# Kernel tuning notes

Hardware: AMD Instinct MI355X
Metric: run time of the kernel (lower is better)

Reference implementation:

```python
import jax, jax.numpy as jnp
import numpy as np

HIDDEN = 1152
NUM_HEADS = 16
HEAD_DIM = HIDDEN // NUM_HEADS  # 72
BATCH, SEQ = 8, 1024


def setup_inputs() -> dict:
    key = jax.random.key(0)
    ks = jax.random.split(key, 9)
    s = 0.02
    return {
        "x": jax.random.normal(ks[0], (BATCH, SEQ, HIDDEN), dtype=jnp.float32),
        "wq": jax.random.normal(ks[1], (HIDDEN, HIDDEN), dtype=jnp.float32) * s,
        "bq": jax.random.normal(ks[2], (HIDDEN,), dtype=jnp.float32) * s,
        "wk": jax.random.normal(ks[3], (HIDDEN, HIDDEN), dtype=jnp.float32) * s,
        "bk": jax.random.normal(ks[4], (HIDDEN,), dtype=jnp.float32) * s,
        "wv": jax.random.normal(ks[5], (HIDDEN, HIDDEN), dtype=jnp.float32) * s,
        "bv": jax.random.normal(ks[6], (HIDDEN,), dtype=jnp.float32) * s,
        "wo": jax.random.normal(ks[7], (HIDDEN, HIDDEN), dtype=jnp.float32) * s,
        "bo": jax.random.normal(ks[8], (HIDDEN,), dtype=jnp.float32) * s,
    }


def reference(x, wq, bq, wk, bk, wv, bv, wo, bo):
    B, S, H = x.shape
    nh, hd = NUM_HEADS, HEAD_DIM
    # projections (weights stored [in, out] to match nn.Linear x @ W^T with W^T precomposed)
    q = (x @ wq + bq).reshape(B, S, nh, hd).transpose(0, 2, 1, 3)  # [B,nh,S,hd]
    k = (x @ wk + bk).reshape(B, S, nh, hd).transpose(0, 2, 1, 3)
    v = (x @ wv + bv).reshape(B, S, nh, hd).transpose(0, 2, 1, 3)
    scale = 1.0 / jnp.sqrt(jnp.asarray(hd, dtype=x.dtype))
    scores = jnp.einsum("bhqd,bhkd->bhqk", q, k) * scale  # [B,nh,S,S]
    attn = jax.nn.softmax(scores, axis=-1)
    out = jnp.einsum("bhqk,bhkd->bhqd", attn, v)  # [B,nh,S,hd]
    out = out.transpose(0, 2, 1, 3).reshape(B, S, H)
    return out @ wo + bo
```

## Files before the change

### kernel.cpp

```cpp
#include <hip/hip_runtime.h>
#include <hip/hip_bf16.h>

#define HIDDEN 1152
#define NUM_HEADS 16
#define BATCH 8
#define SEQ 1024
#define MROWS (BATCH * SEQ)
#define KSTRIDE 104
#define QSCALE_L2E (0.11785113019775793f * 1.4426950408889634f)

typedef __attribute__((ext_vector_type(8))) short short8;
typedef __attribute__((ext_vector_type(4))) float f32x4;

__device__ inline short f2bf(float x) {
  unsigned u = __float_as_uint(x);
  unsigned r = (u + 0x7FFFu + ((u >> 16) & 1u)) >> 16;
  return (short)(r & 0xFFFFu);
}

__device__ inline float fexp2(float x) { return __builtin_exp2f(x); }

__device__ inline void gload16(const void* g, void* l) {
  __builtin_amdgcn_global_load_lds(
      (const __attribute__((address_space(1))) void*)g,
      (__attribute__((address_space(3))) void*)l, 16, 0, 0);
}

__global__ __launch_bounds__(256) void k_prep(const float* __restrict__ X,
                                              short* __restrict__ Xb,
                                              short* __restrict__ Kp,
                                              short* __restrict__ Vt) {
  const int bid = blockIdx.x;
  if (bid < 4608) {
    const size_t base = ((size_t)bid * 256 + threadIdx.x) * 8;
    float4 a = *(const float4*)(X + base);
    float4 b = *(const float4*)(X + base + 4);
    short8 o = {f2bf(a.x), f2bf(a.y), f2bf(a.z), f2bf(a.w),
                f2bf(b.x), f2bf(b.y), f2bf(b.z), f2bf(b.w)};
    *(short8*)(Xb + base) = o;
  } else if (bid < 5120) {
    const int r = (bid - 4608) * 256 + threadIdx.x;
    const short8 z0 = {(short)0xC100, 0, 0, 0, 0, 0, 0, 0};
    const short8 z = {0, 0, 0, 0, 0, 0, 0, 0};
    short* p = Kp + (size_t)r * KSTRIDE + 72;
    *(short8*)(p) = z0;
    *(short8*)(p + 8) = z;
    *(short8*)(p + 16) = z;
  } else {
    const int t = (bid - 5120) * 256 + threadIdx.x;
    const int bh = t >> 10;
    const int off = (t & 1023) * 8;
    const short o = ((t & 1023) >> 7) == 0 ? (short)0x3F80 : (short)0;
    short8 v = {o, o, o, o, o, o, o, o};
    *(short8*)(Vt + (size_t)bh * 81920 + 73728 + off) = v;
  }
}

__global__ __launch_bounds__(256) void k_cvtw(const float* __restrict__ W0,
                                              const float* __restrict__ W1,
                                              const float* __restrict__ W2,
                                              const float* __restrict__ W3,
                                              short* __restrict__ Wt) {
  __shared__ float T[64][65];
  const float* W = (blockIdx.z == 0) ? W0 : (blockIdx.z == 1) ? W1
                 : (blockIdx.z == 2) ? W2 : W3;
  short* dst = Wt + (size_t)blockIdx.z * HIDDEN * HIDDEN;
  const int n0 = blockIdx.x * 64, k0 = blockIdx.y * 64;
  const int tid = threadIdx.x;
  for (int t = tid; t < 4096; t += 256) {
    int r = t >> 6, c = t & 63;
    T[r][c] = W[(size_t)(k0 + r) * HIDDEN + n0 + c];
  }
  __syncthreads();
  for (int t = tid; t < 4096; t += 256) {
    int r = t >> 6, c = t & 63;
    dst[(size_t)(n0 + r) * HIDDEN + k0 + c] = f2bf(T[c][r]);
  }
}

__global__ __launch_bounds__(512) void k_gemm_qkv(
    const short* __restrict__ A, const short* __restrict__ Bt,
    const float* __restrict__ bq, const float* __restrict__ bk,
    const float* __restrict__ bv, short* __restrict__ Qb,
    short* __restrict__ Kp, short* __restrict__ Vt) {
  __shared__ __align__(16) short SM[24576];
  short* As = SM;
  short* Bs = SM + 16384;
  const int tid = threadIdx.x;
  const int lane = tid & 63;
  const int wid = tid >> 6;
  const int wr = wid >> 1, wc = wid & 1;
  const int flat = blockIdx.y * 27 + blockIdx.x;
  const int rid = (flat & 7) * 108 + (flat >> 3);
  const int row0 = (rid / 27) << 8;
  const int colTile = rid % 27;
  const int col0 = colTile << 7;
  const int l15 = lane & 15, lh = lane >> 4;
  const int lr8 = lane >> 3;
  const int csrc = ((lane & 7) ^ lr8) << 3;

  const f32x4 fz = {0.f, 0.f, 0.f, 0.f};
  f32x4 acc[4][4];
#pragma unroll
  for (int m = 0; m < 4; ++m)
#pragma unroll
    for (int n = 0; n < 4; ++n) acc[m][n] = fz;

  for (int k0 = 0; k0 < HIDDEN; k0 += 64) {
#pragma unroll
    for (int i = 0; i < 4; ++i) {
      const int c = (wid << 2) + i;
      const int r = (c << 3) + lr8;
      gload16(A + (size_t)(row0 + r) * HIDDEN + k0 + csrc, (void*)(As + (c << 9)));
    }
#pragma unroll
    for (int i = 0; i < 2; ++i) {
      const int c = (wid << 1) + i;
      const int r = (c << 3) + lr8;
      gload16(Bt + (size_t)(col0 + r) * HIDDEN + k0 + csrc, (void*)(Bs + (c << 9)));
    }
    __syncthreads();
#pragma unroll
    for (int ks = 0; ks < 2; ++ks) {
      short8 af[4], bfr[4];
#pragma unroll
      for (int m = 0; m < 4; ++m) {
        const int r = (wr << 6) + (m << 4) + l15;
        const int off = ((ks << 6) + (lh << 4)) ^ ((r & 7) << 4);
        af[m] = *(const short8*)((const char*)As + r * 128 + off);
      }
#pragma unroll
      for (int n = 0; n < 4; ++n) {
        const int r = (wc << 6) + (n << 4) + l15;
        const int off = ((ks << 6) + (lh << 4)) ^ ((r & 7) << 4);
        bfr[n] = *(const short8*)((const char*)Bs + r * 128 + off);
      }
      __builtin_amdgcn_s_setprio(1);
#pragma unroll
      for (int m = 0; m < 4; ++m)
#pragma unroll
        for (int n = 0; n < 4; ++n)
          acc[m][n] = __builtin_amdgcn_mfma_f32_16x16x32_bf16(af[m], bfr[n], acc[m][n], 0, 0, 0);
      __builtin_amdgcn_s_setprio(0);
    }
    __syncthreads();
  }

  const int cseg = colTile / 9;
  const int cwithin = (colTile % 9) << 7;
  if (cseg < 2) {
    short* dst = (cseg == 0) ? Qb : Kp;
    const float* bias = (cseg == 0) ? bq : bk;
    const float scl = (cseg == 0) ? QSCALE_L2E : 1.0f;
    const int rstride = (cseg == 0) ? 72 : KSTRIDE;
#pragma unroll
    for (int n = 0; n < 4; ++n) {
      const int c = cwithin + (wc << 6) + (n << 4) + l15;
      const int h = c / 72;
      const int d = c - h * 72;
      const float bvx = bias[c];
#pragma unroll
      for (int m = 0; m < 4; ++m)
#pragma unroll
        for (int i = 0; i < 4; ++i) {
          const int r = row0 + (wr << 6) + (m << 4) + (lh << 2) + i;
          const int b = r >> 10, s = r & 1023;
          dst[(size_t)((((b << 4) + h) << 10) + s) * rstride + d] =
              f2bf((acc[m][n][i] + bvx) * scl);
        }
    }
  } else {
    const int b = row0 >> 10;
    const int sb = row0 & 1023;
    short* Td = SM;
#pragma unroll
    for (int p = 0; p < 2; ++p) {
      if (wc == p) {
#pragma unroll
        for (int n = 0; n < 4; ++n) {
          const int ci = n * 16 + l15;
          const float bvx = bv[cwithin + p * 64 + ci];
#pragma unroll
          for (int m = 0; m < 4; ++m) {
            const int r0 = (wr << 6) + (m << 4) + (lh << 2);
            short4 o;
            o.x = f2bf(acc[m][n][0] + bvx);
            o.y = f2bf(acc[m][n][1] + bvx);
            o.z = f2bf(acc[m][n][2] + bvx);
            o.w = f2bf(acc[m][n][3] + bvx);
            *(short4*)(Td + ci * 264 + r0) = o;
          }
        }
      }
      __syncthreads();
      {
        const int ci = tid >> 3;
        const int part = tid & 7;
        const int cg = cwithin + p * 64 + ci;
        const int h = cg / 72;
        const int d = cg - h * 72;
        short* dstp = Vt + (((size_t)(((b << 4) + h) * 80 + d)) << 10) + sb + part * 32;
        const short* srcp = Td + ci * 264 + part * 32;
#pragma unroll
        for (int k = 0; k < 4; ++k)
          *(short8*)(dstp + k * 8) = *(const short8*)(srcp + k * 8);
      }
      __syncthreads();
    }
  }
}

__global__ __launch_bounds__(512) void k_gemm_o(const short* __restrict__ A,
                                                const short* __restrict__ Bt,
                                                const float* __restrict__ bias,
                                                float* __restrict__ C) {
  __shared__ __align__(16) short SM[24576];
  short* As = SM;
  short* Bs = SM + 16384;
  const int tid = threadIdx.x;
  const int lane = tid & 63;
  const int wid = tid >> 6;
  const int wr = wid >> 1, wc = wid & 1;
  const int flat = blockIdx.y * 9 + blockIdx.x;
  const int rid = (flat & 7) * 36 + (flat >> 3);
  const int row0 = (rid / 9) << 8;
  const int col0 = (rid % 9) << 7;
  const int l15 = lane & 15, lh = lane >> 4;
  const int lr8 = lane >> 3;
  const int csrc = ((lane & 7) ^ lr8) << 3;

  const f32x4 fz = {0.f, 0.f, 0.f, 0.f};
  f32x4 acc[4][4];
#pragma unroll
  for (int m = 0; m < 4; ++m)
#pragma unroll
    for (int n = 0; n < 4; ++n) acc[m][n] = fz;

  for (int k0 = 0; k0 < HIDDEN; k0 += 64) {
#pragma unroll
    for (int i = 0; i < 4; ++i) {
      const int c = (wid << 2) + i;
      const int r = (c << 3) + lr8;
      gload16(A + (size_t)(row0 + r) * HIDDEN + k0 + csrc, (void*)(As + (c << 9)));
    }
#pragma unroll
    for (int i = 0; i < 2; ++i) {
      const int c = (wid << 1) + i;
      const int r = (c << 3) + lr8;
      gload16(Bt + (size_t)(col0 + r) * HIDDEN + k0 + csrc, (void*)(Bs + (c << 9)));
    }
    __syncthreads();
#pragma unroll
    for (int ks = 0; ks < 2; ++ks) {
      short8 af[4], bfr[4];
#pragma unroll
      for (int m = 0; m < 4; ++m) {
        const int r = (wr << 6) + (m << 4) + l15;
        const int off = ((ks << 6) + (lh << 4)) ^ ((r & 7) << 4);
        af[m] = *(const short8*)((const char*)As + r * 128 + off);
      }
#pragma unroll
      for (int n = 0; n < 4; ++n) {
        const int r = (wc << 6) + (n << 4) + l15;
        const int off = ((ks << 6) + (lh << 4)) ^ ((r & 7) << 4);
        bfr[n] = *(const short8*)((const char*)Bs + r * 128 + off);
      }
      __builtin_amdgcn_s_setprio(1);
#pragma unroll
      for (int m = 0; m < 4; ++m)
#pragma unroll
        for (int n = 0; n < 4; ++n)
          acc[m][n] = __builtin_amdgcn_mfma_f32_16x16x32_bf16(af[m], bfr[n], acc[m][n], 0, 0, 0);
      __builtin_amdgcn_s_setprio(0);
    }
    __syncthreads();
  }

#pragma unroll
  for (int n = 0; n < 4; ++n) {
    const int c = col0 + (wc << 6) + (n << 4) + l15;
    const float bvx = bias[c];
#pragma unroll
    for (int m = 0; m < 4; ++m)
#pragma unroll
      for (int i = 0; i < 4; ++i) {
        const int r = row0 + (wr << 6) + (m << 4) + (lh << 2) + i;
        C[(size_t)r * HIDDEN + c] = acc[m][n][i] + bvx;
      }
  }
}

__global__ __launch_bounds__(512, 4) void k_attn(const short* __restrict__ Qg,
                                                 const short* __restrict__ Kp,
                                                 const short* __restrict__ Vt,
                                                 short* __restrict__ Og) {
  __shared__ __align__(16) short Ks[64 * KSTRIDE];
  __shared__ __align__(16) short Vs[80 * 64];
  __shared__ __align__(16) short Ps[8 * 16 * 72];
  const int tid = threadIdx.x, lane = tid & 63, wid = tid >> 6;
  const int l15 = lane & 15, lh = lane >> 4;
  const int id = blockIdx.x;
  const int rid = (id & 7) * 64 + (id >> 3);
  const int bh = rid >> 2;
  const int q0 = (rid & 3) << 8;
  const short8 sz = {0, 0, 0, 0, 0, 0, 0, 0};
  const f32x4 fz = {0.f, 0.f, 0.f, 0.f};

  short8 qf[2][3];
#pragma unroll
  for (int m = 0; m < 2; ++m)
#pragma unroll
    for (int ks = 0; ks < 3; ++ks) {
      const int row = q0 + wid * 32 + m * 16 + l15;
      const int e0 = ks * 32 + lh * 8;
      if (e0 < 72)
        qf[m][ks] = *(const short8*)(Qg + ((size_t)bh * 1024 + row) * 72 + e0);
      else if (e0 == 72) {
        short8 v = sz;
        v[0] = (short)0x3F80;
        qf[m][ks] = v;
      } else
        qf[m][ks] = sz;
    }

  f32x4 oacc[2][5];
#pragma unroll
  for (int m = 0; m < 2; ++m)
#pragma unroll
    for (int no = 0; no < 5; ++no) oacc[m][no] = fz;

  const char* kgb = (const char*)Kp + ((size_t)bh * 1024) * (KSTRIDE * 2);
  const char* vgb = (const char*)Vt + (size_t)bh * 163840;
  short* psw = Ps + wid * 1152;

  for (int kt = 0; kt < 16; ++kt) {
    const char* kg = kgb + (size_t)kt * 64 * (KSTRIDE * 2);
    for (int c = wid; c < 13; c += 8)
      gload16(kg + c * 1024 + lane * 16, (char*)Ks + c * 1024);
    for (int c = wid; c < 10; c += 8) {
      const int p = c * 1024 + lane * 16;
      const int d = p >> 7;
      const int sc16 = (lane & 7) ^ (d & 7);
      gload16(vgb + (size_t)d * 2048 + kt * 128 + sc16 * 16, (char*)Vs + c * 1024);
    }
    __syncthreads();

#pragma unroll
    for (int m = 0; m < 2; ++m) {
      f32x4 sa[4];
#pragma unroll
      for (int n = 0; n < 4; ++n) sa[n] = fz;
#pragma unroll
      for (int ks = 0; ks < 3; ++ks) {
        short8 kf[4];
#pragma unroll
        for (int n = 0; n < 4; ++n)
          kf[n] = *(const short8*)((const char*)Ks + (n * 16 + l15) * 208 + ks * 64 + lh * 16);
        __builtin_amdgcn_s_setprio(1);
#pragma unroll
        for (int n = 0; n < 4; ++n)
          sa[n] = __builtin_amdgcn_mfma_f32_16x16x32_bf16(kf[n], qf[m][ks], sa[n], 0, 0, 0);
        __builtin_amdgcn_s_setprio(0);
      }

#pragma unroll
      for (int n = 0; n < 4; ++n)
#pragma unroll
        for (int i = 0; i < 4; ++i) sa[n][i] = fexp2(sa[n][i]);

#pragma unroll
      for (int n = 0; n < 4; ++n) {
        unsigned w0 = __builtin_amdgcn_perm(__float_as_uint(sa[n][1]),
                                            __float_as_uint(sa[n][0]), 0x07060302u);
        unsigned w1 = __builtin_amdgcn_perm(__float_as_uint(sa[n][3]),
                                            __float_as_uint(sa[n][2]), 0x07060302u);
        uint2 w = {w0, w1};
        *(uint2*)((char*)psw + l15 * 144 + n * 32 + lh * 8) = w;
      }

#pragma unroll
      for (int ks = 0; ks < 2; ++ks) {
        const short8 pa = *(const short8*)((const char*)psw + l15 * 144 + ks * 64 + lh * 16);
        short8 vb[5];
        const int cc = ((ks << 2) + lh) ^ (l15 & 7);
#pragma unroll
        for (int no = 0; no < 5; ++no)
          vb[no] = *(const short8*)((const char*)Vs + no * 2048 + l15 * 128 + cc * 16);
        __builtin_amdgcn_s_setprio(1);
#pragma unroll
        for (int no = 0; no < 5; ++no)
          oacc[m][no] = __builtin_amdgcn_mfma_f32_16x16x32_bf16(pa, vb[no], oacc[m][no], 0, 0, 0);
        __builtin_amdgcn_s_setprio(0);
      }
    }
    __syncthreads();
  }

  const int b = bh >> 4, h = bh & 15;
#pragma unroll
  for (int m = 0; m < 2; ++m) {
    float inv[4];
#pragma unroll
    for (int i = 0; i < 4; ++i)
      inv[i] = 1.0f / __shfl(oacc[m][4][i], (lane & 48) + 8);
#pragma unroll
    for (int no = 0; no < 5; ++no) {
      const int d = no * 16 + l15;
      if (d < 72) {
#pragma unroll
        for (int i = 0; i < 4; ++i) {
          const int s = q0 + wid * 32 + m * 16 + lh * 4 + i;
          Og[((size_t)(b * 1024 + s)) * HIDDEN + h * 72 + d] = f2bf(oacc[m][no][i] * inv[i]);
        }
      }
    }
  }
}

extern "C" void kernel_launch(void* const* d_in, const int* in_sizes, int n_in,
                              void* d_out, int out_size, void* d_ws, size_t ws_size,
                              hipStream_t stream) {
  const float* x  = (const float*)d_in[0];
  const float* wq = (const float*)d_in[1];
  const float* bq = (const float*)d_in[2];
  const float* wk = (const float*)d_in[3];
  const float* bk = (const float*)d_in[4];
  const float* wv = (const float*)d_in[5];
  const float* bv = (const float*)d_in[6];
  const float* wo = (const float*)d_in[7];
  const float* bo = (const float*)d_in[8];

  char* ws = (char*)d_ws;
  short* xb = (short*)ws;
  short* wT = (short*)(ws + 18874368);
  short* Qb = (short*)(ws + 29491200);
  short* Kp = (short*)(ws + 48365568);
  short* Vt = (short*)(ws + 75628544);
  const size_t WSZ = (size_t)HIDDEN * HIDDEN;

  k_prep<<<5632, 256, 0, stream>>>(x, xb, Kp, Vt);
  k_cvtw<<<dim3(18, 18, 4), 256, 0, stream>>>(wq, wk, wv, wo, wT);

  k_gemm_qkv<<<dim3(27, 32), 512, 0, stream>>>(xb, wT, bq, bk, bv, Qb, Kp, Vt);
  k_attn<<<512, 512, 0, stream>>>(Qb, Kp, Vt, xb);
  k_gemm_o<<<dim3(9, 32), 512, 0, stream>>>(xb, wT + 3 * WSZ, bo, (float*)d_out);
}
```

Baseline: 190.8 us.

## Double-buffer LDS tiles in QKV and output GEMMs to overlap loads with MFMA

Both GEMM kernels move to dynamic shared memory holding two A/B tile buffers. The next k-tile is prefetched with global_load_lds while MFMAs run on the current tile, and the two barriers per iteration become one. This is meant to hide global-load latency behind compute. The price is doubled LDS per block (96KB), which cuts how many blocks fit on a CU at once.

```diff
diff --git a/kernel.cpp b/kernel.cpp
--- a/kernel.cpp
+++ b/kernel.cpp
@@ -83,9 +83,7 @@
     const float* __restrict__ bq, const float* __restrict__ bk,
     const float* __restrict__ bv, short* __restrict__ Qb,
     short* __restrict__ Kp, short* __restrict__ Vt) {
-  __shared__ __align__(16) short SM[24576];
-  short* As = SM;
-  short* Bs = SM + 16384;
+  extern __shared__ __align__(16) short SM[];
   const int tid = threadIdx.x;
   const int lane = tid & 63;
   const int wid = tid >> 6;
@@ -106,20 +104,42 @@
 #pragma unroll
     for (int n = 0; n < 4; ++n) acc[m][n] = fz;
 
-  for (int k0 = 0; k0 < HIDDEN; k0 += 64) {
-#pragma unroll
-    for (int i = 0; i < 4; ++i) {
-      const int c = (wid << 2) + i;
-      const int r = (c << 3) + lr8;
-      gload16(A + (size_t)(row0 + r) * HIDDEN + k0 + csrc, (void*)(As + (c << 9)));
-    }
-#pragma unroll
-    for (int i = 0; i < 2; ++i) {
-      const int c = (wid << 1) + i;
-      const int r = (c << 3) + lr8;
-      gload16(Bt + (size_t)(col0 + r) * HIDDEN + k0 + csrc, (void*)(Bs + (c << 9)));
-    }
-    __syncthreads();
+#pragma unroll
+  for (int i = 0; i < 4; ++i) {
+    const int c = (wid << 2) + i;
+    const int r = (c << 3) + lr8;
+    gload16(A + (size_t)(row0 + r) * HIDDEN + csrc, (void*)(SM + (c << 9)));
+  }
+#pragma unroll
+  for (int i = 0; i < 2; ++i) {
+    const int c = (wid << 1) + i;
+    const int r = (c << 3) + lr8;
+    gload16(Bt + (size_t)(col0 + r) * HIDDEN + csrc, (void*)(SM + 16384 + (c << 9)));
+  }
+  asm volatile("s_waitcnt vmcnt(0)" ::: "memory");
+  __builtin_amdgcn_s_barrier();
+
+  for (int t = 0; t < 18; ++t) {
+    const int cur = t & 1;
+    const short* Asc = SM + cur * 24576;
+    const short* Bsc = Asc + 16384;
+    if (t < 17) {
+      short* Asn = SM + (cur ^ 1) * 24576;
+      short* Bsn = Asn + 16384;
+      const int k1 = (t + 1) << 6;
+#pragma unroll
+      for (int i = 0; i < 4; ++i) {
+        const int c = (wid << 2) + i;
+        const int r = (c << 3) + lr8;
+        gload16(A + (size_t)(row0 + r) * HIDDEN + k1 + csrc, (void*)(Asn + (c << 9)));
+      }
+#pragma unroll
+      for (int i = 0; i < 2; ++i) {
+        const int c = (wid << 1) + i;
+        const int r = (c << 3) + lr8;
+        gload16(Bt + (size_t)(col0 + r) * HIDDEN + k1 + csrc, (void*)(Bsn + (c << 9)));
+      }
+    }
 #pragma unroll
     for (int ks = 0; ks < 2; ++ks) {
       short8 af[4], bfr[4];
@@ -127,13 +147,13 @@
       for (int m = 0; m < 4; ++m) {
         const int r = (wr << 6) + (m << 4) + l15;
         const int off = ((ks << 6) + (lh << 4)) ^ ((r & 7) << 4);
-        af[m] = *(const short8*)((const char*)As + r * 128 + off);
+        af[m] = *(const short8*)((const char*)Asc + r * 128 + off);
       }
 #pragma unroll
       for (int n = 0; n < 4; ++n) {
         const int r = (wc << 6) + (n << 4) + l15;
         const int off = ((ks << 6) + (lh << 4)) ^ ((r & 7) << 4);
-        bfr[n] = *(const short8*)((const char*)Bs + r * 128 + off);
+        bfr[n] = *(const short8*)((const char*)Bsc + r * 128 + off);
       }
       __builtin_amdgcn_s_setprio(1);
 #pragma unroll
@@ -143,7 +163,8 @@
           acc[m][n] = __builtin_amdgcn_mfma_f32_16x16x32_bf16(af[m], bfr[n], acc[m][n], 0, 0, 0);
       __builtin_amdgcn_s_setprio(0);
     }
-    __syncthreads();
+    asm volatile("s_waitcnt vmcnt(0) lgkmcnt(0)" ::: "memory");
+    __builtin_amdgcn_s_barrier();
   }
 
   const int cseg = colTile / 9;
@@ -214,9 +235,7 @@
                                                 const short* __restrict__ Bt,
                                                 const float* __restrict__ bias,
                                                 float* __restrict__ C) {
-  __shared__ __align__(16) short SM[24576];
-  short* As = SM;
-  short* Bs = SM + 16384;
+  extern __shared__ __align__(16) short SM[];
   const int tid = threadIdx.x;
   const int lane = tid & 63;
   const int wid = tid >> 6;
@@ -236,20 +255,42 @@
 #pragma unroll
     for (int n = 0; n < 4; ++n) acc[m][n] = fz;
 
-  for (int k0 = 0; k0 < HIDDEN; k0 += 64) {
-#pragma unroll
-    for (int i = 0; i < 4; ++i) {
-      const int c = (wid << 2) + i;
-      const int r = (c << 3) + lr8;
-      gload16(A + (size_t)(row0 + r) * HIDDEN + k0 + csrc, (void*)(As + (c << 9)));
-    }
-#pragma unroll
-    for (int i = 0; i < 2; ++i) {
-      const int c = (wid << 1) + i;
-      const int r = (c << 3) + lr8;
-      gload16(Bt + (size_t)(col0 + r) * HIDDEN + k0 + csrc, (void*)(Bs + (c << 9)));
-    }
-    __syncthreads();
+#pragma unroll
+  for (int i = 0; i < 4; ++i) {
+    const int c = (wid << 2) + i;
+    const int r = (c << 3) + lr8;
+    gload16(A + (size_t)(row0 + r) * HIDDEN + csrc, (void*)(SM + (c << 9)));
+  }
+#pragma unroll
+  for (int i = 0; i < 2; ++i) {
+    const int c = (wid << 1) + i;
+    const int r = (c << 3) + lr8;
+    gload16(Bt + (size_t)(col0 + r) * HIDDEN + csrc, (void*)(SM + 16384 + (c << 9)));
+  }
+  asm volatile("s_waitcnt vmcnt(0)" ::: "memory");
+  __builtin_amdgcn_s_barrier();
+
+  for (int t = 0; t < 18; ++t) {
+    const int cur = t & 1;
+    const short* Asc = SM + cur * 24576;
+    const short* Bsc = Asc + 16384;
+    if (t < 17) {
+      short* Asn = SM + (cur ^ 1) * 24576;
+      short* Bsn = Asn + 16384;
+      const int k1 = (t + 1) << 6;
+#pragma unroll
+      for (int i = 0; i < 4; ++i) {
+        const int c = (wid << 2) + i;
+        const int r = (c << 3) + lr8;
+        gload16(A + (size_t)(row0 + r) * HIDDEN + k1 + csrc, (void*)(Asn + (c << 9)));
+      }
+#pragma unroll
+      for (int i = 0; i < 2; ++i) {
+        const int c = (wid << 1) + i;
+        const int r = (c << 3) + lr8;
+        gload16(Bt + (size_t)(col0 + r) * HIDDEN + k1 + csrc, (void*)(Bsn + (c << 9)));
+      }
+    }
 #pragma unroll
     for (int ks = 0; ks < 2; ++ks) {
       short8 af[4], bfr[4];
@@ -257,13 +298,13 @@
       for (int m = 0; m < 4; ++m) {
         const int r = (wr << 6) + (m << 4) + l15;
         const int off = ((ks << 6) + (lh << 4)) ^ ((r & 7) << 4);
-        af[m] = *(const short8*)((const char*)As + r * 128 + off);
+        af[m] = *(const short8*)((const char*)Asc + r * 128 + off);
       }
 #pragma unroll
       for (int n = 0; n < 4; ++n) {
         const int r = (wc << 6) + (n << 4) + l15;
         const int off = ((ks << 6) + (lh << 4)) ^ ((r & 7) << 4);
-        bfr[n] = *(const short8*)((const char*)Bs + r * 128 + off);
+        bfr[n] = *(const short8*)((const char*)Bsc + r * 128 + off);
       }
       __builtin_amdgcn_s_setprio(1);
 #pragma unroll
@@ -273,7 +314,8 @@
           acc[m][n] = __builtin_amdgcn_mfma_f32_16x16x32_bf16(af[m], bfr[n], acc[m][n], 0, 0, 0);
       __builtin_amdgcn_s_setprio(0);
     }
-    __syncthreads();
+    asm volatile("s_waitcnt vmcnt(0) lgkmcnt(0)" ::: "memory");
+    __builtin_amdgcn_s_barrier();
   }
 
 #pragma unroll
@@ -438,10 +480,19 @@
   short* Vt = (short*)(ws + 75628544);
   const size_t WSZ = (size_t)HIDDEN * HIDDEN;
 
+  static int lds_ok = 0;
+  if (!lds_ok) {
+    hipFuncSetAttribute((const void*)k_gemm_qkv,
+                        hipFuncAttributeMaxDynamicSharedMemorySize, 98304);
+    hipFuncSetAttribute((const void*)k_gemm_o,
+                        hipFuncAttributeMaxDynamicSharedMemorySize, 98304);
+    lds_ok = 1;
+  }
+
   k_prep<<<5632, 256, 0, stream>>>(x, xb, Kp, Vt);
   k_cvtw<<<dim3(18, 18, 4), 256, 0, stream>>>(wq, wk, wv, wo, wT);
 
-  k_gemm_qkv<<<dim3(27, 32), 512, 0, stream>>>(xb, wT, bq, bk, bv, Qb, Kp, Vt);
+  k_gemm_qkv<<<dim3(27, 32), 512, 98304, stream>>>(xb, wT, bq, bk, bv, Qb, Kp, Vt);
   k_attn<<<512, 512, 0, stream>>>(Qb, Kp, Vt, xb);
-  k_gemm_o<<<dim3(9, 32), 512, 0, stream>>>(xb, wT + 3 * WSZ, bo, (float*)d_out);
-}
+  k_gemm_o<<<dim3(9, 32), 512, 98304, stream>>>(xb, wT + 3 * WSZ, bo, (float*)d_out);
+}
```

After: 211.9 us. 1.11x slower.

## Double-buffer QKV GEMM shared-memory tiles with K-step of 32

Applied to the files above, without the earlier changes.

Restructures the QKV projection GEMM main loop to use two shared-memory buffers with a K-step of 32 instead of a single buffer with K-step 64. The next tile's global-to-LDS loads are issued before computing on the current tile, with an explicit vmcnt wait and raw barriers, so memory latency overlaps with MFMA work. The LDS swizzle is changed to suit the 64-byte row layout. This doubles the number of loop iterations and barriers, and the hand-written vmcnt counts must match the number of issued loads.

```diff
diff --git a/kernel.cpp b/kernel.cpp
--- a/kernel.cpp
+++ b/kernel.cpp
@@ -84,8 +84,6 @@
     const float* __restrict__ bv, short* __restrict__ Qb,
     short* __restrict__ Kp, short* __restrict__ Vt) {
   __shared__ __align__(16) short SM[24576];
-  short* As = SM;
-  short* Bs = SM + 16384;
   const int tid = threadIdx.x;
   const int lane = tid & 63;
   const int wid = tid >> 6;
@@ -96,8 +94,9 @@
   const int colTile = rid % 27;
   const int col0 = colTile << 7;
   const int l15 = lane & 15, lh = lane >> 4;
-  const int lr8 = lane >> 3;
-  const int csrc = ((lane & 7) ^ lr8) << 3;
+  const int rl = lane >> 2;
+  const int s16 = (lane & 3) ^ ((lane >> 3) & 3);
+  const int fslot = lh ^ ((l15 >> 1) & 3);
 
   const f32x4 fz = {0.f, 0.f, 0.f, 0.f};
   f32x4 acc[4][4];
@@ -106,45 +105,54 @@
 #pragma unroll
     for (int n = 0; n < 4; ++n) acc[m][n] = fz;
 
-  for (int k0 = 0; k0 < HIDDEN; k0 += 64) {
-#pragma unroll
-    for (int i = 0; i < 4; ++i) {
-      const int c = (wid << 2) + i;
-      const int r = (c << 3) + lr8;
-      gload16(A + (size_t)(row0 + r) * HIDDEN + k0 + csrc, (void*)(As + (c << 9)));
-    }
-#pragma unroll
-    for (int i = 0; i < 2; ++i) {
-      const int c = (wid << 1) + i;
-      const int r = (c << 3) + lr8;
-      gload16(Bt + (size_t)(col0 + r) * HIDDEN + k0 + csrc, (void*)(Bs + (c << 9)));
-    }
-    __syncthreads();
-#pragma unroll
-    for (int ks = 0; ks < 2; ++ks) {
-      short8 af[4], bfr[4];
-#pragma unroll
-      for (int m = 0; m < 4; ++m) {
-        const int r = (wr << 6) + (m << 4) + l15;
-        const int off = ((ks << 6) + (lh << 4)) ^ ((r & 7) << 4);
-        af[m] = *(const short8*)((const char*)As + r * 128 + off);
-      }
-#pragma unroll
-      for (int n = 0; n < 4; ++n) {
-        const int r = (wc << 6) + (n << 4) + l15;
-        const int off = ((ks << 6) + (lh << 4)) ^ ((r & 7) << 4);
-        bfr[n] = *(const short8*)((const char*)Bs + r * 128 + off);
-      }
-      __builtin_amdgcn_s_setprio(1);
-#pragma unroll
-      for (int m = 0; m < 4; ++m)
-#pragma unroll
-        for (int n = 0; n < 4; ++n)
-          acc[m][n] = __builtin_amdgcn_mfma_f32_16x16x32_bf16(af[m], bfr[n], acc[m][n], 0, 0, 0);
-      __builtin_amdgcn_s_setprio(0);
-    }
-    __syncthreads();
-  }
+#define STAGE_QKV(dst, kk)                                                     \
+  {                                                                            \
+    short* As_ = (dst);                                                        \
+    short* Bs_ = (dst) + 8192;                                                 \
+    _Pragma("unroll") for (int i = 0; i < 2; ++i) {                            \
+      const int c = (wid << 1) + i;                                            \
+      gload16(A + (size_t)(row0 + (c << 4) + rl) * HIDDEN + (kk) + (s16 << 3), \
+              (void*)(As_ + (c << 9)));                                        \
+    }                                                                          \
+    gload16(Bt + (size_t)(col0 + (wid << 4) + rl) * HIDDEN + (kk) + (s16 << 3),\
+            (void*)(Bs_ + (wid << 9)));                                        \
+  }
+
+  STAGE_QKV(SM, 0);
+
+  for (int t = 0; t < 36; ++t) {
+    const short* Asc = SM + (t & 1) * 12288;
+    const short* Bsc = Asc + 8192;
+    if (t < 35) {
+      short* nxt = SM + ((t + 1) & 1) * 12288;
+      STAGE_QKV(nxt, (t + 1) << 5);
+      asm volatile("s_waitcnt vmcnt(3)" ::: "memory");
+    } else {
+      asm volatile("s_waitcnt vmcnt(0)" ::: "memory");
+    }
+    __builtin_amdgcn_s_barrier();
+
+    short8 af[4], bfr[4];
+#pragma unroll
+    for (int m = 0; m < 4; ++m) {
+      const int r = (wr << 6) + (m << 4) + l15;
+      af[m] = *(const short8*)(Asc + r * 32 + (fslot << 3));
+    }
+#pragma unroll
+    for (int n = 0; n < 4; ++n) {
+      const int r = (wc << 6) + (n << 4) + l15;
+      bfr[n] = *(const short8*)(Bsc + r * 32 + (fslot << 3));
+    }
+    __builtin_amdgcn_s_setprio(1);
+#pragma unroll
+    for (int m = 0; m < 4; ++m)
+#pragma unroll
+      for (int n = 0; n < 4; ++n)
+        acc[m][n] = __builtin_amdgcn_mfma_f32_16x16x32_bf16(af[m], bfr[n], acc[m][n], 0, 0, 0);
+    __builtin_amdgcn_s_setprio(0);
+    __builtin_amdgcn_s_barrier();
+  }
+#undef STAGE_QKV
 
   const int cseg = colTile / 9;
   const int cwithin = (colTile % 9) << 7;
```

Measured after the change: 199.2 us. 1.04x slower.

## Double-buffer K/V tiles in attention kernel with async prefetch

Applied to the files above, without the earlier changes.

The attention kernel moves K and V tiles into two dynamic-LDS buffers and prefetches the next tile with global_load_lds while the current one is computed. It synchronises with explicit vmcnt waits and raw barriers instead of __syncthreads. LDS use roughly doubles to 66 KB per block, so launch bounds drop to 2 blocks per CU and occupancy falls. The hipFuncSetAttribute call runs only once, guarded by a static flag.

```diff
diff --git a/kernel.cpp b/kernel.cpp
--- a/kernel.cpp
+++ b/kernel.cpp
@@ -290,13 +290,11 @@
   }
 }
 
-__global__ __launch_bounds__(512, 4) void k_attn(const short* __restrict__ Qg,
+__global__ __launch_bounds__(512, 2) void k_attn(const short* __restrict__ Qg,
                                                  const short* __restrict__ Kp,
                                                  const short* __restrict__ Vt,
                                                  short* __restrict__ Og) {
-  __shared__ __align__(16) short Ks[64 * KSTRIDE];
-  __shared__ __align__(16) short Vs[80 * 64];
-  __shared__ __align__(16) short Ps[8 * 16 * 72];
+  extern __shared__ __align__(16) short SMD[];
   const int tid = threadIdx.x, lane = tid & 63, wid = tid >> 6;
   const int l15 = lane & 15, lh = lane >> 4;
   const int id = blockIdx.x;
@@ -331,19 +329,43 @@
 
   const char* kgb = (const char*)Kp + ((size_t)bh * 1024) * (KSTRIDE * 2);
   const char* vgb = (const char*)Vt + (size_t)bh * 163840;
-  short* psw = Ps + wid * 1152;
+  short* psw = SMD + 24576 + wid * 1152;
+
+#define STAGE_ATTN(buf, t)                                                    \
+  {                                                                           \
+    const char* kg_ = kgb + (size_t)(t) * 13312;                              \
+    short* ksb_ = SMD + (buf) * 6656;                                         \
+    short* vsb_ = SMD + 13312 + (buf) * 5632;                                 \
+    _Pragma("unroll") for (int i = 0; i < 3; ++i) {                           \
+      const int c = wid + (i << 3);                                           \
+      if (c < 13) {                                                           \
+        gload16(kg_ + c * 1024 + lane * 16, (char*)ksb_ + c * 1024);          \
+      } else {                                                                \
+        const int cv = c - 13;                                                \
+        const int cvc = cv > 9 ? 9 : cv;                                      \
+        const int p = cvc * 1024 + lane * 16;                                 \
+        const int d = p >> 7;                                                 \
+        const int sc16 = (lane & 7) ^ (d & 7);                                \
+        gload16(vgb + (size_t)d * 2048 + (t) * 128 + sc16 * 16,               \
+                (char*)vsb_ + cv * 1024);                                     \
+      }                                                                       \
+    }                                                                         \
+  }
+
+  STAGE_ATTN(0, 0);
 
   for (int kt = 0; kt < 16; ++kt) {
-    const char* kg = kgb + (size_t)kt * 64 * (KSTRIDE * 2);
-    for (int c = wid; c < 13; c += 8)
-      gload16(kg + c * 1024 + lane * 16, (char*)Ks + c * 1024);
-    for (int c = wid; c < 10; c += 8) {
-      const int p = c * 1024 + lane * 16;
-      const int d = p >> 7;
-      const int sc16 = (lane & 7) ^ (d & 7);
-      gload16(vgb + (size_t)d * 2048 + kt * 128 + sc16 * 16, (char*)Vs + c * 1024);
-    }
-    __syncthreads();
+    const int cur = kt & 1;
+    if (kt < 15) {
+      STAGE_ATTN(cur ^ 1, kt + 1);
+      asm volatile("s_waitcnt vmcnt(3)" ::: "memory");
+    } else {
+      asm volatile("s_waitcnt vmcnt(0)" ::: "memory");
+    }
+    __builtin_amdgcn_s_barrier();
+
+    const short* Ksc = SMD + cur * 6656;
+    const short* Vsc = SMD + 13312 + cur * 5632;
 
 #pragma unroll
     for (int m = 0; m < 2; ++m) {
@@ -355,7 +377,7 @@
         short8 kf[4];
 #pragma unroll
         for (int n = 0; n < 4; ++n)
-          kf[n] = *(const short8*)((const char*)Ks + (n * 16 + l15) * 208 + ks * 64 + lh * 16);
+          kf[n] = *(const short8*)((const char*)Ksc + (n * 16 + l15) * 208 + ks * 64 + lh * 16);
         __builtin_amdgcn_s_setprio(1);
 #pragma unroll
         for (int n = 0; n < 4; ++n)
@@ -385,7 +407,7 @@
         const int cc = ((ks << 2) + lh) ^ (l15 & 7);
 #pragma unroll
         for (int no = 0; no < 5; ++no)
-          vb[no] = *(const short8*)((const char*)Vs + no * 2048 + l15 * 128 + cc * 16);
+          vb[no] = *(const short8*)((const char*)Vsc + no * 2048 + l15 * 128 + cc * 16);
         __builtin_amdgcn_s_setprio(1);
 #pragma unroll
         for (int no = 0; no < 5; ++no)
@@ -393,8 +415,9 @@
         __builtin_amdgcn_s_setprio(0);
       }
     }
-    __syncthreads();
-  }
+    __builtin_amdgcn_s_barrier();
+  }
+#undef STAGE_ATTN
 
   const int b = bh >> 4, h = bh & 15;
 #pragma unroll
@@ -438,10 +461,17 @@
   short* Vt = (short*)(ws + 75628544);
   const size_t WSZ = (size_t)HIDDEN * HIDDEN;
 
+  static int lds_ok = 0;
+  if (!lds_ok) {
+    hipFuncSetAttribute((const void*)k_attn,
+                        hipFuncAttributeMaxDynamicSharedMemorySize, 67584);
+    lds_ok = 1;
+  }
+
   k_prep<<<5632, 256, 0, stream>>>(x, xb, Kp, Vt);
   k_cvtw<<<dim3(18, 18, 4), 256, 0, stream>>>(wq, wk, wv, wo, wT);
 
   k_gemm_qkv<<<dim3(27, 32), 512, 0, stream>>>(xb, wT, bq, bk, bv, Qb, Kp, Vt);
-  k_attn<<<512, 512, 0, stream>>>(Qb, Kp, Vt, xb);
+  k_attn<<<512, 512, 67584, stream>>>(Qb, Kp, Vt, xb);
   k_gemm_o<<<dim3(9, 32), 512, 0, stream>>>(xb, wT + 3 * WSZ, bo, (float*)d_out);
 }
```

New measurement: 200.6 us. 5.2% more time.
